# Optimization experiments

Hardware: AMD Instinct MI355X
Metric: run time of the kernel (lower is better)

## Reference

```python
import jax, jax.numpy as jnp
import numpy as np

N = 100_000      # nodes
E = 1_600_000    # edges (avg degree 16)
D = 128          # emb_dim
L = 2            # num_layer
BN_EPS = 1e-5


def setup_inputs() -> dict:
    key = jax.random.key(0)
    ks = jax.random.split(key, 16)
    s = 0.05
    inp = {
        # int inputs
        "x": jax.random.randint(ks[0], (N, 9), 0, 2),
        "z": jax.random.randint(ks[1], (N,), 0, 1000),
        "edge_index": jax.random.randint(ks[2], (2, E), 0, N),
        "edge_attr": jax.random.randint(ks[3], (E, 3), 0, 2),
        # learned params
        "atom_emb": jax.random.normal(ks[4], (9, 119, D), jnp.float32) * s,  # padded stacked AtomEncoder tables
        "z_emb": jax.random.normal(ks[5], (1000, D), jnp.float32) * s,
        "bond_emb": jax.random.normal(ks[6], (L, 3, 6, D), jnp.float32) * s,  # padded BondEncoder tables per layer
        "eps": jnp.zeros((L,), jnp.float32),
        "W1": jax.random.normal(ks[7], (L, D, 2 * D), jnp.float32) * s,
        "b1": jnp.zeros((L, 2 * D), jnp.float32),
        "g1": jnp.ones((L, 2 * D), jnp.float32),
        "be1": jnp.zeros((L, 2 * D), jnp.float32),
        "W2": jax.random.normal(ks[8], (L, 2 * D, D), jnp.float32) * s,
        "b2": jnp.zeros((L, D), jnp.float32),
        "bng": jnp.ones((L, D), jnp.float32),
        "bnb": jnp.zeros((L, D), jnp.float32),
    }
    return inp


def _batchnorm(h, g, b):
    # training-mode BatchNorm1d: batch stats, biased variance
    m = h.mean(axis=0)
    v = h.var(axis=0)
    return (h - m) * jax.lax.rsqrt(v + BN_EPS) * g + b


def _multi_embed(tables, idx):
    # tables: [F, V, D], idx: [N, F] -> sum_f tables[f][idx[:, f]]  -> [N, D]
    return jax.vmap(lambda t, i: t[i], in_axes=(0, 1))(tables, idx).sum(axis=0)


def reference(x, z, edge_index, edge_attr, atom_emb, z_emb, bond_emb, eps,
              W1, b1, g1, be1, W2, b2, bng, bnb):
    src, dst = edge_index[0], edge_index[1]
    # h0 = AtomEncoder(x) + z_embedding(z)
    h = _multi_embed(atom_emb, x) + z_emb[z]
    for l in range(L):
        # GINConv: bond encode -> gather -> relu message -> scatter-add -> MLP
        e_emb = _multi_embed(bond_emb[l], edge_attr)          # [E, D]
        msg = jax.nn.relu(h[src] + e_emb)                      # [E, D]
        agg = jax.ops.segment_sum(msg, dst, num_segments=N)    # [N, D]
        pre = (1.0 + eps[l]) * h + agg
        hid = jax.nn.relu(_batchnorm(pre @ W1[l] + b1[l], g1[l], be1[l]))
        hconv = hid @ W2[l] + b2[l]
        h = _batchnorm(hconv, bng[l], bnb[l])
        if l < L - 1:
            h = jax.nn.relu(h)   # dropout ratio 0 -> identity
    return h
```

## Files before the change

### kernel.cpp

```cpp
#include <hip/hip_runtime.h>

#define D 128
#define BN_EPS 1e-5f
#define NSUB 1024
#define CAP2 2048

typedef __attribute__((ext_vector_type(8))) short short8;
typedef __attribute__((ext_vector_type(4))) float floatx4;

__device__ __forceinline__ float bf2f(unsigned short u) {
    unsigned int x = ((unsigned int)u) << 16;
    return __builtin_bit_cast(float, x);
}
__device__ __forceinline__ unsigned short f2bf(float f) {
    unsigned int x = __builtin_bit_cast(unsigned int, f);
    x = x + 0x7FFFu + ((x >> 16) & 1u);
    return (unsigned short)(x >> 16);
}
__device__ __forceinline__ int magdiv(unsigned int x, unsigned long long magic) {
    return (int)(((unsigned long long)x * magic) >> 44);
}

__global__ __launch_bounds__(256)
void setup_kernel(const int* __restrict__ x, const int* __restrict__ z,
                  const float* __restrict__ atom_emb, const float* __restrict__ z_emb,
                  unsigned short* __restrict__ hb, int N, int nbNode,
                  const float* __restrict__ bond_emb, unsigned short* __restrict__ comb,
                  const float* __restrict__ W1, unsigned short* __restrict__ w1p,
                  const float* __restrict__ W2, unsigned short* __restrict__ w2p) {
    const int b = blockIdx.x;
    const int tid = threadIdx.x;
    if (b < nbNode) {
        int gid = b * 256 + tid;
        int node = gid >> 5;
        if (node >= N) return;
        int d0 = (gid & 31) * 4;
        float4 acc = *(const float4*)(z_emb + (size_t)z[node] * D + d0);
#pragma unroll
        for (int f = 0; f < 9; ++f) {
            int v = x[node * 9 + f];
            const float4 t = *(const float4*)(atom_emb + (size_t)(f * 119 + v) * D + d0);
            acc.x += t.x; acc.y += t.y; acc.z += t.z; acc.w += t.w;
        }
        ushort4 o;
        o.x = f2bf(acc.x); o.y = f2bf(acc.y); o.z = f2bf(acc.z); o.w = f2bf(acc.w);
        *(ushort4*)(hb + (size_t)node * D + d0) = o;
    } else if (b < nbNode + 216) {
        int t = (b - nbNode) * 256 + tid;
        int layer = t / (216 * D);
        int idx = t - layer * (216 * D);
        int c = idx >> 7, d = idx & 127;
        int a0 = c / 36, a1 = (c / 6) % 6, a2 = c % 6;
        const float* bb = bond_emb + (size_t)layer * 3 * 6 * D;
        float v = bb[(0 * 6 + a0) * D + d] + bb[(1 * 6 + a1) * D + d] + bb[(2 * 6 + a2) * D + d];
        comb[(size_t)layer * 216 * D + idx] = f2bf(v);
    } else {
        int isW2 = (b >= nbNode + 216 + 256);
        int t = (b - nbNode - 216 - (isW2 ? 256 : 0)) * 256 + tid;
        int layer = t >> 15;
        int idx = t & 32767;
        int logN = isW2 ? 7 : 8;
        int NCOLS = 1 << logN;
        int k = idx >> logN, n = idx & (NCOLS - 1);
        int k0 = k >> 5, kq = k & 31, q = kq >> 3, j = kq & 7;
        int tt = n >> 4, ln = n & 15;
        size_t dest = (((size_t)k0 * (NCOLS >> 4) + tt) << 9) + ((q << 4) + ln) * 8 + j;
        const float* W = (isW2 ? W2 : W1) + (size_t)layer * 32768;
        unsigned short* Wp = (isW2 ? w2p : w1p) + (size_t)layer * 32768;
        Wp[dest] = f2bf(W[idx]);
    }
}

__global__ __launch_bounds__(256)
void partition_kernel(const int* __restrict__ ei, const int* __restrict__ ea,
                      unsigned int* __restrict__ subL, int* __restrict__ tail2,
                      int E, int N, unsigned long long magic, int ntiles, int nblocks) {
    __shared__ int lcnt[1024], lbase[1024];
    const int tid = threadIdx.x;
    for (int tile = blockIdx.x; tile < ntiles; tile += nblocks) {
        const int tb = tile * 4096;
#pragma unroll
        for (int i = 0; i < 4; ++i) lcnt[tid + i * 256] = 0;
        __syncthreads();
        int sub[16];
        unsigned int entry[16];
#pragma unroll
        for (int j = 0; j < 16; ++j) {
            int e = tb + j * 256 + tid;
            if (e < E) {
                int dst = ei[E + e];
                int c = (ea[3 * e] * 6 + ea[3 * e + 1]) * 6 + ea[3 * e + 2];
                int k = magdiv((unsigned)dst * 1024u, magic);
                int lo = (int)(((long long)k * N + 1023) >> 10);
                sub[j] = k;
                entry[j] = (unsigned int)ei[e] | ((unsigned int)c << 17) |
                           ((unsigned int)(dst - lo) << 25);
                atomicAdd(&lcnt[k], 1);
            } else {
                sub[j] = -1;
            }
        }
        __syncthreads();
#pragma unroll
        for (int i = 0; i < 4; ++i) {
            int k = tid + i * 256;
            int c = lcnt[k];
            if (c) lbase[k] = atomicAdd(&tail2[k], c);
            lcnt[k] = 0;
        }
        __syncthreads();
#pragma unroll
        for (int j = 0; j < 16; ++j) {
            if (sub[j] >= 0) {
                int k = sub[j];
                int pos = lbase[k] + atomicAdd(&lcnt[k], 1);
                if (pos < CAP2) subL[(size_t)k * CAP2 + pos] = entry[j];
            }
        }
        __syncthreads();
    }
}

__global__ __launch_bounds__(1024)
void subscan_kernel(const int* __restrict__ tail2, int* __restrict__ subbase,
                    int* __restrict__ offsets, int N) {
    const int tid = threadIdx.x, lane = tid & 63, wid = tid >> 6;
    int v = min(tail2[tid], CAP2);
    int s = v;
#pragma unroll
    for (int off = 1; off < 64; off <<= 1) {
        int t = __shfl_up(s, off, 64);
        if (lane >= off) s += t;
    }
    __shared__ int ws[16];
    if (lane == 63) ws[wid] = s;
    __syncthreads();
    if (wid == 0) {
        int w = (lane < 16) ? ws[lane] : 0;
#pragma unroll
        for (int off = 1; off < 16; off <<= 1) {
            int t = __shfl_up(w, off, 64);
            if (lane >= off) w += t;
        }
        if (lane < 16) ws[lane] = w;
    }
    __syncthreads();
    int excl = (wid ? ws[wid - 1] : 0) + s - v;
    subbase[tid] = excl;
    if (tid == 1023) offsets[N] = excl + v;
}

__global__ __launch_bounds__(256)
void csr_sort_kernel(const unsigned int* __restrict__ subL, const int* __restrict__ tail2,
                     const int* __restrict__ subbase, int* __restrict__ offsets,
                     int* __restrict__ bucket, int N) {
    const int k = blockIdx.x;
    const int tid = threadIdx.x, lane = tid & 63, wid = tid >> 6;
    const int len = min(tail2[k], CAP2);
    const int base = subbase[k];
    const int lo = (int)(((long long)k * N + 1023) >> 10);
    const int hi = (int)(((long long)(k + 1) * N + 1023) >> 10);
    const int nn = hi - lo;
    __shared__ int cnt[128], loff[128], wsum[4];
    __shared__ unsigned int sorted[CAP2];
    const unsigned int* src = subL + (size_t)k * CAP2;

    if (tid < 128) cnt[tid] = 0;
    __syncthreads();
    for (int i = tid; i < len; i += 256) atomicAdd(&cnt[src[i] >> 25], 1);
    __syncthreads();
    int v = (tid < 128) ? cnt[tid] : 0;
    int s = v;
#pragma unroll
    for (int off = 1; off < 64; off <<= 1) {
        int t = __shfl_up(s, off, 64);
        if (lane >= off) s += t;
    }
    if (lane == 63) wsum[wid] = s;
    __syncthreads();
    if (tid < 128) loff[tid] = ((wid == 1) ? wsum[0] : 0) + s - v;
    __syncthreads();
    if (tid < nn) offsets[lo + tid] = base + loff[tid];
    if (tid < 128) cnt[tid] = 0;
    __syncthreads();
    for (int i = tid; i < len; i += 256) {
        unsigned int e = src[i];
        int ld = e >> 25;
        int pos = loff[ld] + atomicAdd(&cnt[ld], 1);
        sorted[pos] = e & 0x1FFFFFFu;
    }
    __syncthreads();
    for (int i = tid; i < len; i += 256) bucket[base + i] = (int)sorted[i];
}

__global__ __launch_bounds__(256)
void gather_reduce_kernel(const int* __restrict__ offsets, const int* __restrict__ bucket,
                          const unsigned short* __restrict__ comb,
                          const unsigned short* __restrict__ hb,
                          const float* __restrict__ eps_l,
                          unsigned short* __restrict__ pre, int N) {
    const int node = (blockIdx.x * 256 + threadIdx.x) >> 6;
    if (node >= N) return;
    const int lane = threadIdx.x & 63;
    const int q = lane >> 4, ln = lane & 15;
    const int d0 = ln * 8;

    union U8 { int4 i; unsigned short u[8]; };
    const int beg = offsets[node], end = offsets[node + 1];

    float a[8];
#pragma unroll
    for (int j = 0; j < 8; ++j) a[j] = 0.f;

    for (int base = beg; base < end; base += 8) {
        int e0 = base + q;
        int e1 = base + 4 + q;
        int pk0 = bucket[min(e0, end - 1)];
        int pk1 = bucket[min(e1, end - 1)];
        U8 h0, c0, h1, c1;
        h0.i = *(const int4*)(hb + (size_t)(pk0 & 0x1FFFF) * D + d0);
        c0.i = *(const int4*)(comb + (size_t)(pk0 >> 17) * D + d0);
        h1.i = *(const int4*)(hb + (size_t)(pk1 & 0x1FFFF) * D + d0);
        c1.i = *(const int4*)(comb + (size_t)(pk1 >> 17) * D + d0);
        if (e0 < end) {
#pragma unroll
            for (int j = 0; j < 8; ++j) a[j] += fmaxf(bf2f(h0.u[j]) + bf2f(c0.u[j]), 0.0f);
        }
        if (e1 < end) {
#pragma unroll
            for (int j = 0; j < 8; ++j) a[j] += fmaxf(bf2f(h1.u[j]) + bf2f(c1.u[j]), 0.0f);
        }
    }
#pragma unroll
    for (int j = 0; j < 8; ++j) {
        a[j] += __shfl_xor(a[j], 16, 64);
        a[j] += __shfl_xor(a[j], 32, 64);
    }
    if (q == 0) {
        const float s = 1.0f + eps_l[0];
        U8 hv; hv.i = *(const int4*)(hb + (size_t)node * D + d0);
        U8 o;
#pragma unroll
        for (int j = 0; j < 8; ++j) o.u[j] = f2bf(a[j] + s * bf2f(hv.u[j]));
        *(int4*)(pre + (size_t)node * D + d0) = o.i;
    }
}

template <int K, int NCOLS, int TRANSFORM, int OUTBF>
__global__ __launch_bounds__(256)
void mfma_gemm_kernel(const unsigned short* __restrict__ A,
                      const unsigned short* __restrict__ Wp,
                      const float* __restrict__ bias,
                      const float* __restrict__ tscale, const float* __restrict__ tshift,
                      unsigned short* __restrict__ Cbf, float* __restrict__ Cf,
                      float* __restrict__ partial, int M) {
    constexpr int NT = NCOLS / 16;
    constexpr int NCHUNK = K / 32;
    constexpr int CPP = NCHUNK / 2;
    __shared__ unsigned short Ws[16384];
    __shared__ float red[NCOLS * 2];

    const int tid = threadIdx.x;
    const int wave = tid >> 6, lane = tid & 63;
    const int quad = lane >> 4, ln = lane & 15;
    const int m_base = blockIdx.x * 64 + wave * 16;
    int arow = m_base + ln;
    if (arow >= M) arow = M - 1;
    const int kq = quad * 8;

    int4 araw[NCHUNK];
#pragma unroll
    for (int c = 0; c < NCHUNK; ++c)
        araw[c] = *(const int4*)(A + (size_t)arow * K + c * 32 + kq);

    for (int i = tid; i < NCOLS * 2; i += 256) red[i] = 0.f;

    floatx4 acc[NT];
#pragma unroll
    for (int t = 0; t < NT; ++t) acc[t] = (floatx4){0.f, 0.f, 0.f, 0.f};

#pragma unroll
    for (int ph = 0; ph < 2; ++ph) {
        if (ph) __syncthreads();
#pragma unroll
        for (int i = 0; i < 16384; i += 2048)
            *(int4*)&Ws[i + tid * 8] = *(const int4*)&Wp[ph * 16384 + i + tid * 8];
        __syncthreads();
#pragma unroll
        for (int cc = 0; cc < CPP; ++cc) {
            const int c = ph * CPP + cc;
            short8 afrag;
            if constexpr (TRANSFORM) {
                union { int4 i; unsigned short u[8]; } raw;
                raw.i = araw[c];
                const int kb = c * 32 + kq;
                float4 sc0 = *(const float4*)(tscale + kb);
                float4 sc1 = *(const float4*)(tscale + kb + 4);
                float4 sh0 = *(const float4*)(tshift + kb);
                float4 sh1 = *(const float4*)(tshift + kb + 4);
                union { short8 v; unsigned short u[8]; } au;
                au.u[0] = f2bf(fmaxf(bf2f(raw.u[0]) * sc0.x + sh0.x, 0.f));
                au.u[1] = f2bf(fmaxf(bf2f(raw.u[1]) * sc0.y + sh0.y, 0.f));
                au.u[2] = f2bf(fmaxf(bf2f(raw.u[2]) * sc0.z + sh0.z, 0.f));
                au.u[3] = f2bf(fmaxf(bf2f(raw.u[3]) * sc0.w + sh0.w, 0.f));
                au.u[4] = f2bf(fmaxf(bf2f(raw.u[4]) * sc1.x + sh1.x, 0.f));
                au.u[5] = f2bf(fmaxf(bf2f(raw.u[5]) * sc1.y + sh1.y, 0.f));
                au.u[6] = f2bf(fmaxf(bf2f(raw.u[6]) * sc1.z + sh1.z, 0.f));
                au.u[7] = f2bf(fmaxf(bf2f(raw.u[7]) * sc1.w + sh1.w, 0.f));
                afrag = au.v;
            } else {
                afrag = __builtin_bit_cast(short8, araw[c]);
            }
#pragma unroll
            for (int t = 0; t < NT; ++t) {
                short8 bfrag = *(const short8*)&Ws[(((cc * NT) + t) << 9) + lane * 8];
                acc[t] = __builtin_amdgcn_mfma_f32_16x16x32_bf16(afrag, bfrag, acc[t], 0, 0, 0);
            }
        }
    }

#pragma unroll
    for (int t = 0; t < NT; ++t) {
        int col = t * 16 + ln;
        float bv = bias[col];
        float sv = 0.f, qv = 0.f;
#pragma unroll
        for (int r = 0; r < 4; ++r) {
            int row = m_base + quad * 4 + r;
            if (row < M) {
                float v = acc[t][r] + bv;
                sv += v; qv += v * v;
                if constexpr (OUTBF) Cbf[(size_t)row * NCOLS + col] = f2bf(v);
                else                 Cf[(size_t)row * NCOLS + col] = v;
            }
        }
        sv += __shfl_xor(sv, 16, 64); sv += __shfl_xor(sv, 32, 64);
        qv += __shfl_xor(qv, 16, 64); qv += __shfl_xor(qv, 32, 64);
        if (quad == 0) {
            atomicAdd(&red[col], sv);
            atomicAdd(&red[NCOLS + col], qv);
        }
    }
    __syncthreads();
    float* pout = partial + (size_t)blockIdx.x * (NCOLS * 2);
    for (int i = tid; i < NCOLS * 2; i += 256) pout[i] = red[i];
}

template <int NCOLS>
__global__ __launch_bounds__(256)
void reduce_stats_kernel(const float* __restrict__ partial, int nb,
                         const float* __restrict__ g, const float* __restrict__ b,
                         float* __restrict__ scale, float* __restrict__ shift, float invN) {
    const int col = blockIdx.x;
    const int tid = threadIdx.x;
    float s = 0.f, q = 0.f;
    for (int bb = tid; bb < nb; bb += 256) {
        const float* p = partial + (size_t)bb * (NCOLS * 2);
        s += p[col];
        q += p[NCOLS + col];
    }
#pragma unroll
    for (int off = 32; off > 0; off >>= 1) {
        s += __shfl_xor(s, off, 64);
        q += __shfl_xor(q, off, 64);
    }
    __shared__ float ws[4], wq[4];
    if ((tid & 63) == 0) { ws[tid >> 6] = s; wq[tid >> 6] = q; }
    __syncthreads();
    if (tid == 0) {
        s = ws[0] + ws[1] + ws[2] + ws[3];
        q = wq[0] + wq[1] + wq[2] + wq[3];
        float mean = s * invN;
        float var = q * invN - mean * mean;
        float inv = 1.0f / sqrtf(var + BN_EPS);
        float sc = g[col] * inv;
        scale[col] = sc;
        shift[col] = b[col] - mean * sc;
    }
}

__global__ void bn_apply_kernel(const unsigned short* __restrict__ Xb,
                                float* __restrict__ Yf, unsigned short* __restrict__ Yb,
                                const float* __restrict__ scale, const float* __restrict__ shift,
                                int N, int mode) {
    int gid = blockIdx.x * blockDim.x + threadIdx.x;
    int node = gid >> 5;
    if (node >= N) return;
    int d0 = (gid & 31) * 4;
    ushort4 b = *(const ushort4*)(Xb + (size_t)node * D + d0);
    float4 v;
    v.x = bf2f(b.x); v.y = bf2f(b.y); v.z = bf2f(b.z); v.w = bf2f(b.w);
    float4 sc = *(const float4*)(scale + d0);
    float4 sh = *(const float4*)(shift + d0);
    float4 o;
    o.x = v.x * sc.x + sh.x;
    o.y = v.y * sc.y + sh.y;
    o.z = v.z * sc.z + sh.z;
    o.w = v.w * sc.w + sh.w;
    if (mode == 0) {
        ushort4 ob;
        ob.x = f2bf(fmaxf(o.x, 0.f));
        ob.y = f2bf(fmaxf(o.y, 0.f));
        ob.z = f2bf(fmaxf(o.z, 0.f));
        ob.w = f2bf(fmaxf(o.w, 0.f));
        *(ushort4*)(Yb + (size_t)node * D + d0) = ob;
    } else {
        *(float4*)(Yf + (size_t)node * D + d0) = o;
    }
}

extern "C" void kernel_launch(void* const* d_in, const int* in_sizes, int n_in,
                              void* d_out, int out_size, void* d_ws, size_t ws_size,
                              hipStream_t stream) {
    const int*   x        = (const int*)d_in[0];
    const int*   z        = (const int*)d_in[1];
    const int*   ei       = (const int*)d_in[2];
    const int*   ea       = (const int*)d_in[3];
    const float* atom_emb = (const float*)d_in[4];
    const float* z_emb    = (const float*)d_in[5];
    const float* bond_emb = (const float*)d_in[6];
    const float* eps      = (const float*)d_in[7];
    const float* W1       = (const float*)d_in[8];
    const float* b1       = (const float*)d_in[9];
    const float* g1       = (const float*)d_in[10];
    const float* be1      = (const float*)d_in[11];
    const float* W2       = (const float*)d_in[12];
    const float* b2       = (const float*)d_in[13];
    const float* bng      = (const float*)d_in[14];
    const float* bnb      = (const float*)d_in[15];

    const int N = in_sizes[1];
    const int E = in_sizes[3] / 3;

    float* h = (float*)d_out;

    const int ngb = (N + 63) / 64;
    const unsigned long long magic = ((1ULL << 44) / (unsigned int)N) + 1;

    char* ws = (char*)d_ws;
    size_t off = 0;
    auto alloc = [&](size_t bytes) { void* p = ws + off; off += (bytes + 255) & ~(size_t)255; return p; };
    unsigned short* pre_bf = (unsigned short*)alloc((size_t)N * D * 2);
    unsigned short* out2_bf = pre_bf;
    unsigned short* out1_bf = (unsigned short*)alloc((size_t)N * 2 * D * 2);
    unsigned short* hb      = (unsigned short*)alloc((size_t)N * D * 2);
    int* offsets = (int*)alloc((size_t)(N + 1) * 4);
    int* bucket  = (int*)alloc((size_t)E * 4);
    unsigned int* subL = (unsigned int*)alloc((size_t)NSUB * CAP2 * 4);
    int* subbase = (int*)alloc(NSUB * 4);
    float* stats = (float*)alloc(1024 * 4);
    float* partial1 = (float*)alloc((size_t)ngb * 512 * 4);
    float* partial2 = (float*)alloc((size_t)ngb * 256 * 4);
    unsigned short* w1p  = (unsigned short*)alloc((size_t)2 * D * 2 * D * 2);
    unsigned short* w2p  = (unsigned short*)alloc((size_t)2 * 2 * D * D * 2);
    unsigned short* comb = (unsigned short*)alloc((size_t)2 * 216 * D * 2);
    int* tail2 = (int*)out1_bf;

    float* scale1 = stats;
    float* shift1 = stats + 256;
    float* scale2 = stats + 512;
    float* shift2 = stats + 640;

    const float invN = 1.0f / (float)N;
    const int ntiles = (E + 4095) / 4096;
    const int nbNode = (N * 32 + 255) / 256;

    hipMemsetAsync(tail2, 0, NSUB * sizeof(int), stream);
    partition_kernel<<<256, 256, 0, stream>>>(ei, ea, subL, tail2, E, N, magic, ntiles, 256);
    subscan_kernel<<<1, 1024, 0, stream>>>(tail2, subbase, offsets, N);
    csr_sort_kernel<<<NSUB, 256, 0, stream>>>(subL, tail2, subbase, offsets, bucket, N);

    setup_kernel<<<nbNode + 216 + 256 + 256, 256, 0, stream>>>(
        x, z, atom_emb, z_emb, hb, N, nbNode, bond_emb, comb, W1, w1p, W2, w2p);

    for (int l = 0; l < 2; ++l) {
        gather_reduce_kernel<<<(N * 64 + 255) / 256, 256, 0, stream>>>(
            offsets, bucket, comb + (size_t)l * 216 * D, hb, eps + l, pre_bf, N);

        mfma_gemm_kernel<128, 256, 0, 1><<<ngb, 256, 0, stream>>>(
            pre_bf, w1p + (size_t)l * D * 2 * D, b1 + (size_t)l * 2 * D,
            nullptr, nullptr, out1_bf, nullptr, partial1, N);
        reduce_stats_kernel<256><<<256, 256, 0, stream>>>(
            partial1, ngb, g1 + (size_t)l * 2 * D, be1 + (size_t)l * 2 * D,
            scale1, shift1, invN);

        mfma_gemm_kernel<256, 128, 1, 1><<<ngb, 256, 0, stream>>>(
            out1_bf, w2p + (size_t)l * 2 * D * D, b2 + (size_t)l * D,
            scale1, shift1, out2_bf, nullptr, partial2, N);
        reduce_stats_kernel<128><<<128, 256, 0, stream>>>(
            partial2, ngb, bng + (size_t)l * D, bnb + (size_t)l * D,
            scale2, shift2, invN);

        bn_apply_kernel<<<(N * 32 + 255) / 256, 256, 0, stream>>>(
            out2_bf, h, hb, scale2, shift2, N, l == 0 ? 0 : 1);
    }
}
```

Baseline: 558.3 us.

## Use 16 lanes per node in gather-reduce and keep combined bond table in fp32

The gather-reduce kernel now assigns 16 threads per node instead of 64. Each thread walks all of the node's edges in steps of four, with four independent gathers in flight, which removes the cross-lane shuffle reduction and the idle lanes. The combined bond-embedding table is now stored in fp32, which removes the bf16 rounding of edge embeddings and doubles the table's read size, though the table is small enough to stay cached. The self term is folded into the accumulator initialisation, and the launch grid shrinks to match.

Result: faster. 537.9 us (-3.6%).

```diff
diff --git a/kernel.cpp b/kernel.cpp
--- a/kernel.cpp
+++ b/kernel.cpp
@@ -25,7 +25,7 @@
 void setup_kernel(const int* __restrict__ x, const int* __restrict__ z,
                   const float* __restrict__ atom_emb, const float* __restrict__ z_emb,
                   unsigned short* __restrict__ hb, int N, int nbNode,
-                  const float* __restrict__ bond_emb, unsigned short* __restrict__ comb,
+                  const float* __restrict__ bond_emb, float* __restrict__ comb,
                   const float* __restrict__ W1, unsigned short* __restrict__ w1p,
                   const float* __restrict__ W2, unsigned short* __restrict__ w2p) {
     const int b = blockIdx.x;
@@ -53,7 +53,7 @@
         int a0 = c / 36, a1 = (c / 6) % 6, a2 = c % 6;
         const float* bb = bond_emb + (size_t)layer * 3 * 6 * D;
         float v = bb[(0 * 6 + a0) * D + d] + bb[(1 * 6 + a1) * D + d] + bb[(2 * 6 + a2) * D + d];
-        comb[(size_t)layer * 216 * D + idx] = f2bf(v);
+        comb[(size_t)layer * 216 * D + idx] = v;
     } else {
         int isW2 = (b >= nbNode + 216 + 256);
         int t = (b - nbNode - 216 - (isW2 ? 256 : 0)) * 256 + tid;
@@ -195,55 +195,64 @@
 
 __global__ __launch_bounds__(256)
 void gather_reduce_kernel(const int* __restrict__ offsets, const int* __restrict__ bucket,
-                          const unsigned short* __restrict__ comb,
+                          const float* __restrict__ comb,
                           const unsigned short* __restrict__ hb,
                           const float* __restrict__ eps_l,
                           unsigned short* __restrict__ pre, int N) {
-    const int node = (blockIdx.x * 256 + threadIdx.x) >> 6;
+    int gid = blockIdx.x * blockDim.x + threadIdx.x;
+    int node = gid >> 4;
     if (node >= N) return;
-    const int lane = threadIdx.x & 63;
-    const int q = lane >> 4, ln = lane & 15;
-    const int d0 = ln * 8;
+    int d0 = (gid & 15) * 8;
 
     union U8 { int4 i; unsigned short u[8]; };
+    union C8 { float4 v[2]; float f[8]; };
+    float s = 1.0f + eps_l[0];
+    float a[8];
+    {
+        U8 hv; hv.i = *(const int4*)(hb + (size_t)node * D + d0);
+#pragma unroll
+        for (int j = 0; j < 8; ++j) a[j] = bf2f(hv.u[j]) * s;
+    }
     const int beg = offsets[node], end = offsets[node + 1];
-
-    float a[8];
-#pragma unroll
-    for (int j = 0; j < 8; ++j) a[j] = 0.f;
-
-    for (int base = beg; base < end; base += 8) {
-        int e0 = base + q;
-        int e1 = base + 4 + q;
-        int pk0 = bucket[min(e0, end - 1)];
-        int pk1 = bucket[min(e1, end - 1)];
-        U8 h0, c0, h1, c1;
+    for (int p = beg; p < end; p += 4) {
+        int rem = end - p;
+        int pk0 = bucket[p];
+        int pk1 = bucket[rem > 1 ? p + 1 : p];
+        int pk2 = bucket[rem > 2 ? p + 2 : p];
+        int pk3 = bucket[rem > 3 ? p + 3 : p];
+        U8 h0, h1, h2, h3;
+        C8 c0, c1, c2, c3;
         h0.i = *(const int4*)(hb + (size_t)(pk0 & 0x1FFFF) * D + d0);
-        c0.i = *(const int4*)(comb + (size_t)(pk0 >> 17) * D + d0);
+        c0.v[0] = *(const float4*)(comb + (size_t)(pk0 >> 17) * D + d0);
+        c0.v[1] = *(const float4*)(comb + (size_t)(pk0 >> 17) * D + d0 + 4);
         h1.i = *(const int4*)(hb + (size_t)(pk1 & 0x1FFFF) * D + d0);
-        c1.i = *(const int4*)(comb + (size_t)(pk1 >> 17) * D + d0);
-        if (e0 < end) {
-#pragma unroll
-            for (int j = 0; j < 8; ++j) a[j] += fmaxf(bf2f(h0.u[j]) + bf2f(c0.u[j]), 0.0f);
-        }
-        if (e1 < end) {
-#pragma unroll
-            for (int j = 0; j < 8; ++j) a[j] += fmaxf(bf2f(h1.u[j]) + bf2f(c1.u[j]), 0.0f);
-        }
-    }
-#pragma unroll
-    for (int j = 0; j < 8; ++j) {
-        a[j] += __shfl_xor(a[j], 16, 64);
-        a[j] += __shfl_xor(a[j], 32, 64);
-    }
-    if (q == 0) {
-        const float s = 1.0f + eps_l[0];
-        U8 hv; hv.i = *(const int4*)(hb + (size_t)node * D + d0);
-        U8 o;
-#pragma unroll
-        for (int j = 0; j < 8; ++j) o.u[j] = f2bf(a[j] + s * bf2f(hv.u[j]));
-        *(int4*)(pre + (size_t)node * D + d0) = o.i;
-    }
+        c1.v[0] = *(const float4*)(comb + (size_t)(pk1 >> 17) * D + d0);
+        c1.v[1] = *(const float4*)(comb + (size_t)(pk1 >> 17) * D + d0 + 4);
+        h2.i = *(const int4*)(hb + (size_t)(pk2 & 0x1FFFF) * D + d0);
+        c2.v[0] = *(const float4*)(comb + (size_t)(pk2 >> 17) * D + d0);
+        c2.v[1] = *(const float4*)(comb + (size_t)(pk2 >> 17) * D + d0 + 4);
+        h3.i = *(const int4*)(hb + (size_t)(pk3 & 0x1FFFF) * D + d0);
+        c3.v[0] = *(const float4*)(comb + (size_t)(pk3 >> 17) * D + d0);
+        c3.v[1] = *(const float4*)(comb + (size_t)(pk3 >> 17) * D + d0 + 4);
+#pragma unroll
+        for (int j = 0; j < 8; ++j) a[j] += fmaxf(bf2f(h0.u[j]) + c0.f[j], 0.0f);
+        if (rem > 1) {
+#pragma unroll
+            for (int j = 0; j < 8; ++j) a[j] += fmaxf(bf2f(h1.u[j]) + c1.f[j], 0.0f);
+        }
+        if (rem > 2) {
+#pragma unroll
+            for (int j = 0; j < 8; ++j) a[j] += fmaxf(bf2f(h2.u[j]) + c2.f[j], 0.0f);
+        }
+        if (rem > 3) {
+#pragma unroll
+            for (int j = 0; j < 8; ++j) a[j] += fmaxf(bf2f(h3.u[j]) + c3.f[j], 0.0f);
+        }
+    }
+    U8 o;
+#pragma unroll
+    for (int j = 0; j < 8; ++j) o.u[j] = f2bf(a[j]);
+    *(int4*)(pre + (size_t)node * D + d0) = o.i;
 }
 
 template <int K, int NCOLS, int TRANSFORM, int OUTBF>
@@ -453,7 +462,7 @@
     float* partial2 = (float*)alloc((size_t)ngb * 256 * 4);
     unsigned short* w1p  = (unsigned short*)alloc((size_t)2 * D * 2 * D * 2);
     unsigned short* w2p  = (unsigned short*)alloc((size_t)2 * 2 * D * D * 2);
-    unsigned short* comb = (unsigned short*)alloc((size_t)2 * 216 * D * 2);
+    float* comb = (float*)alloc((size_t)2 * 216 * D * 4);
     int* tail2 = (int*)out1_bf;
 
     float* scale1 = stats;
@@ -474,7 +483,7 @@
         x, z, atom_emb, z_emb, hb, N, nbNode, bond_emb, comb, W1, w1p, W2, w2p);
 
     for (int l = 0; l < 2; ++l) {
-        gather_reduce_kernel<<<(N * 64 + 255) / 256, 256, 0, stream>>>(
+        gather_reduce_kernel<<<(N * 16 + 255) / 256, 256, 0, stream>>>(
             offsets, bucket, comb + (size_t)l * 216 * D, hb, eps + l, pre_bf, N);
 
         mfma_gemm_kernel<128, 256, 0, 1><<<ngb, 256, 0, stream>>>(
```
